# Performance work log

Hardware: AMD Instinct MI355X
Metric: run time of the kernel (lower is better)

## Reference

```python
import jax, jax.numpy as jnp
import numpy as np

NUM_HEAD = 16
NUM_SEQ = 2048
NUM_FEAT = 1024
HEAD_DIM = NUM_FEAT // NUM_HEAD
LN_EPS = 1e-5


def _constants():
    # decay per head: log(1 - 2^{-5-h})
    decay = jnp.log(1.0 - 2.0 ** (-5.0 - jnp.arange(NUM_HEAD, dtype=jnp.float32)))
    idx = jnp.arange(NUM_SEQ, dtype=jnp.float32)
    diff = idx[:, None] - idx[None, :]                      # [s, s]
    # exp(diff * decay) on lower triangle (incl. diagonal), 0 above
    mask = jnp.where(diff[None] >= 0, jnp.exp(diff[None] * decay[:, None, None]), 0.0)  # [h, s, s]
    # rotary angles: each frequency repeated twice
    angle = 1.0 / 10000.0 ** jnp.linspace(0.0, 1.0, HEAD_DIM // 2)
    angle = jnp.repeat(angle, 2)                            # [hd]
    sin = jnp.sin(idx[:, None] * angle[None, :])            # [s, hd]
    cos = jnp.cos(idx[:, None] * angle[None, :])
    return mask, sin, cos


def _rotate_every_two(x):
    x1 = x[..., ::2]
    x2 = x[..., 1::2]
    return jnp.stack((-x2, x1), axis=-1).reshape(x.shape)


def setup_inputs() -> dict:
    key = jax.random.key(0)
    ks = jax.random.split(key, 5)
    b, s, d = 4, NUM_SEQ, NUM_FEAT
    x = jax.random.normal(ks[0], (b, s, d), dtype=jnp.float32)
    Wq = jax.random.normal(ks[1], (d, d), dtype=jnp.float32) * 0.02
    Wk = jax.random.normal(ks[2], (d, d), dtype=jnp.float32) * 0.02
    Wv = jax.random.normal(ks[3], (d, d), dtype=jnp.float32) * 0.02
    Wo = jax.random.normal(ks[4], (d, d), dtype=jnp.float32) * 0.02
    ln_w = jnp.ones((HEAD_DIM,), dtype=jnp.float32)
    ln_b = jnp.zeros((HEAD_DIM,), dtype=jnp.float32)
    return {"x": x, "Wq": Wq, "Wk": Wk, "Wv": Wv, "Wo": Wo, "ln_w": ln_w, "ln_b": ln_b}


def reference(x, Wq, Wk, Wv, Wo, ln_w, ln_b):
    b, s, d = x.shape
    h, hd = NUM_HEAD, HEAD_DIM
    mask, sin, cos = _constants()

    def proj(W):
        # torch Linear (no bias): x @ W.T -> [b, h, s, hd]
        return (x @ W.T).reshape(b, s, h, hd).transpose(0, 2, 1, 3)

    q, k, v = proj(Wq), proj(Wk), proj(Wv)
    # rotary theta shift (sin/cos broadcast over batch & head)
    q = q * cos + _rotate_every_two(q) * sin
    k = k * cos + _rotate_every_two(k) * sin

    r = jnp.einsum('bhsd,bhtd->bhst', q, k) * mask[None]    # decay-masked scores
    o = jnp.einsum('bhst,bhtd->bhsd', r, v)                 # [b, h, s, hd]

    # LayerNorm over head_dim
    mu = jnp.mean(o, axis=-1, keepdims=True)
    var = jnp.var(o, axis=-1, keepdims=True)
    y = (o - mu) * jax.lax.rsqrt(var + LN_EPS) * ln_w + ln_b

    y = y.transpose(0, 2, 1, 3).reshape(b, s, d)
    return jax.nn.silu(y) @ Wo.T
```

## Files before the change

### kernel.cpp

```cpp
#include <hip/hip_runtime.h>
#include <math.h>

typedef unsigned short u16;
typedef __attribute__((ext_vector_type(8))) short short8;
typedef __attribute__((ext_vector_type(4))) float floatx4;

#define LDS_AS(p) ((__attribute__((address_space(3))) void*)(p))
#define GLB_AS(p) ((const __attribute__((address_space(1))) void*)(p))

__device__ __forceinline__ u16 f2bf(float f) {
  unsigned int u = __float_as_uint(f);
  u += 0x7fffu + ((u >> 16) & 1u);
  return (u16)(u >> 16);
}

__device__ __forceinline__ void gld16(const void* g, void* l) {
  __builtin_amdgcn_global_load_lds(GLB_AS(g), LDS_AS(l), 16, 0, 0);
}

__device__ __forceinline__ floatx4 mfma16(short8 a, short8 b, floatx4 c) {
  return __builtin_amdgcn_mfma_f32_16x16x32_bf16(a, b, c, 0, 0, 0);
}


__global__ void prep_kernel(const float* __restrict__ x, const float* __restrict__ Wq,
                            const float* __restrict__ Wk, const float* __restrict__ Wv,
                            const float* __restrict__ Wo, u16* __restrict__ xp,
                            u16* __restrict__ wqkvp, u16* __restrict__ wop,
                            float2* __restrict__ rtab) {
  int i = blockIdx.x * blockDim.x + threadIdx.x;
  const int str = gridDim.x * blockDim.x;
  for (; i < 3211264; i += str) {
    if (i < 3145728) {
      int U; u16* d;
      const float* s;
      if (i < 2097152)      { U = i;           d = xp;    s = x;  }
      else if (i < 2883584) { U = i - 2097152; d = wqkvp; s = nullptr; }
      else                  { U = i - 2883584; d = wop;   s = Wo; }
      const int tile = U >> 12;
      const int kc   = (U >> 7) & 31;
      const int lane = (U >> 1) & 63;
      const int jh   = U & 1;
      const int scol = kc * 32 + (lane >> 4) * 8 + jh * 4;
      int srow = tile * 16 + (lane & 15);
      if (s == nullptr) {
        const int sel = srow >> 10;
        srow &= 1023;
        s = (sel == 0) ? Wq : (sel == 1) ? Wk : Wv;
      }
      float4 v = ((const float4*)s)[srow * 256 + (scol >> 2)];
      ushort4 o;
      o.x = f2bf(v.x); o.y = f2bf(v.y); o.z = f2bf(v.z); o.w = f2bf(v.w);
      ((ushort4*)d)[U] = o;
    } else {
      const int t = i - 3145728;
      const int seq = t >> 5, dh = t & 31;
      const float freq = exp2f(-(float)dh * 0.42863594770f);
      float sn, cs;
      __sincosf((float)seq * freq, &sn, &cs);
      rtab[t] = make_float2(sn, cs);
    }
  }
}

template <int EPI>
__global__ __launch_bounds__(256, 2)
void gemm_bt(const u16* __restrict__ A, const u16* __restrict__ Bw, int K,
             u16* __restrict__ qb, u16* __restrict__ kb, u16* __restrict__ vtb,
             u16* __restrict__ kwt, const float2* __restrict__ rtab,
             float* __restrict__ outp) {
  constexpr int AP   = (EPI == 0) ? 8 : 4;
  constexpr int BUFU = (AP + 16) * 512;
  constexpr int AOFF = AP * 512;
  constexpr int AI   = (EPI == 0) ? 8 : 4;
  constexpr int IH   = (EPI == 0) ? 2 : 1;
  __shared__ __align__(16) u16 smem[3 * 12288];
  const int tid = threadIdx.x;
  const int w = tid >> 6, lane = tid & 63;
  const int quad = lane >> 4, l15 = lane & 15;
  const int m0 = blockIdx.y * (EPI == 0 ? 128 : 64), n0 = blockIdx.x * 256;

  const size_t tsz = (size_t)(K >> 5) * 512;
  const u16* A0 = A + ((size_t)(m0 >> 4) + (EPI == 0 ? 2 * w : w)) * tsz + lane * 8;
  const u16* A1 = A0 + tsz;
  const u16* Bb = Bw + ((size_t)(n0 >> 4) + 4 * w) * tsz + lane * 8;

  auto stage = [&](int buf, int kc) {
    const int nb = buf * BUFU;
    gld16(A0 + (size_t)kc * 512, &smem[nb + (EPI == 0 ? 2 * w : w) * 512]);
    if constexpr (EPI == 0)
      gld16(A1 + (size_t)kc * 512, &smem[nb + (2 * w + 1) * 512]);
#pragma unroll
    for (int e = 0; e < 4; ++e)
      gld16(Bb + (size_t)e * tsz + (size_t)kc * 512,
            &smem[nb + AOFF + (4 * w + e) * 512]);
  };

  floatx4 acc[AI][4] = {};
  const int NT = K >> 5;

  stage(0, 0);
  stage(1, 1);
  if constexpr (EPI == 0)
    asm volatile("s_waitcnt vmcnt(6)" ::: "memory");
  else
    asm volatile("s_waitcnt vmcnt(5)" ::: "memory");
  __builtin_amdgcn_s_barrier();

  int cur = 0, stg = 2;
  for (int t = 0; t < NT; ++t) {
    const u16* Ap = &smem[cur * BUFU];
    const u16* Bp = Ap + AOFF;
    short8 a[AI], b[4];
#pragma unroll
    for (int i = 0; i < AI; ++i)
      a[i] = *(const short8*)&Ap[i * 512 + lane * 8];
#pragma unroll
    for (int j = 0; j < 4; ++j)
      b[j] = *(const short8*)&Bp[(w * 4 + j) * 512 + lane * 8];
    if (t + 2 < NT) {
      stage(stg, t + 2);
      if constexpr (EPI == 0)
        asm volatile("s_waitcnt vmcnt(6)" ::: "memory");
      else
        asm volatile("s_waitcnt vmcnt(5)" ::: "memory");
    } else {
      asm volatile("s_waitcnt vmcnt(0)" ::: "memory");
    }
    __builtin_amdgcn_s_barrier();
    asm volatile("s_waitcnt lgkmcnt(0)" ::: "memory");
    __builtin_amdgcn_sched_barrier(0);
    __builtin_amdgcn_s_setprio(1);
#pragma unroll
    for (int i = 0; i < AI; ++i)
#pragma unroll
      for (int j = 0; j < 4; ++j)
        acc[i][j] = mfma16(a[i], b[j], acc[i][j]);
    __builtin_amdgcn_s_setprio(0);
    asm volatile("" ::: "memory");
    __builtin_amdgcn_s_barrier();
    asm volatile("" ::: "memory");
    cur = (cur == 2) ? 0 : cur + 1;
    stg = (stg == 2) ? 0 : stg + 1;
  }

  u16* scr = &smem[w * 4096];

  const int ncb = n0 + w * 64;

#pragma unroll
  for (int ih = 0; ih < IH; ++ih) {
    const int mrb = m0 + ih * 64;

    if (EPI == 0) {
      const int which = n0 >> 10;
      const int c1024 = ncb & 1023;
      const int bidx = mrb >> 11;
      const int hh = c1024 >> 6;
      const int seq0 = mrb & 2047;
      const int chk = seq0 >> 7;

      if (which < 2) {
#pragma unroll
        for (int j = 0; j < 4; ++j) {
          const int d = j * 16 + l15;
          const int dc = d >> 3, dl = d & 7;
#pragma unroll
          for (int i = 0; i < 4; ++i)
#pragma unroll
            for (int r = 0; r < 4; ++r) {
              const int sl = i * 16 + quad * 4 + r;
              const int seq = seq0 + sl;
              const float v = acc[ih * 4 + i][j][r];
              const float p = __shfl_xor(v, 1, 64);
              const float2 sc = rtab[(d >> 1) + seq * 32];
              const float res = (d & 1) ? (v * sc.y + p * sc.x) : (v * sc.y - p * sc.x);
              scr[sl * 64 + (((dc + (sl >> 2)) & 7) << 3) + dl] = f2bf(res);
            }
        }
        u16* dst = ((which == 0) ? qb : kb) +
                   (((size_t)(bidx * 16 + hh) * 16 + chk) << 13);
#pragma unroll
        for (int nl = 0; nl < 4; ++nl)
#pragma unroll
          for (int kk2 = 0; kk2 < 2; ++kk2) {
            const int slr = nl * 16 + l15;
            const int slot = ((kk2 * 4 + quad) + (slr >> 2)) & 7;
            short8 vv = *(const short8*)&scr[slr * 64 + slot * 8];
            *(short8*)(dst + (((ih * 4 + nl) * 2 + kk2) * 512) + lane * 8) = vv;
          }
        if (which == 1) {
          const float l2h = __log2f(1.0f - exp2f(-(float)(5 + hh)));
#pragma unroll
          for (int j = 0; j < 4; ++j) {
            const int d = j * 16 + l15;
#pragma unroll
            for (int i = 0; i < 4; ++i) {
              ushort4 pk;
#pragma unroll
              for (int r = 0; r < 4; ++r) {
                const int sl = i * 16 + quad * 4 + r;
                const int seq = seq0 + sl;
                const float v = acc[ih * 4 + i][j][r];
                const float p = __shfl_xor(v, 1, 64);
                const float2 sc = rtab[(d >> 1) + seq * 32];
                const float res = (d & 1) ? (v * sc.y + p * sc.x) : (v * sc.y - p * sc.x);
                const float wgt = exp2f((float)(127 - (seq & 127)) * l2h);
                ((u16*)&pk)[r] = f2bf(res * wgt);
              }
              *(ushort4*)&scr[d * 64 + ((i * 16 + quad * 4 + 8 * (d & 7)) & 63)] = pk;
            }
          }
          u16* dw = kwt + (((size_t)(bidx * 16 + hh) * 16 + chk) << 13);
#pragma unroll
          for (int m = 0; m < 4; ++m)
#pragma unroll
            for (int ks2 = 0; ks2 < 2; ++ks2) {
              const int dr = m * 16 + l15;
              const int col = ((ks2 * 32 + quad * 8) + 8 * (dr & 7)) & 63;
              short8 vv = *(const short8*)&scr[dr * 64 + col];
              *(short8*)(dw + ((m * 4 + ih * 2 + ks2) * 512) + lane * 8) = vv;
            }
        }
      } else {
#pragma unroll
        for (int j = 0; j < 4; ++j) {
          const int d = j * 16 + l15;
#pragma unroll
          for (int i = 0; i < 4; ++i) {
            ushort4 pk;
            pk.x = f2bf(acc[ih * 4 + i][j][0]);
            pk.y = f2bf(acc[ih * 4 + i][j][1]);
            pk.z = f2bf(acc[ih * 4 + i][j][2]);
            pk.w = f2bf(acc[ih * 4 + i][j][3]);
            *(ushort4*)&scr[d * 64 + ((i * 16 + quad * 4 + 8 * (d & 7)) & 63)] = pk;
          }
        }
        u16* dh = vtb + (((size_t)(bidx * 16 + hh) * 16 + chk) << 13);
#pragma unroll
        for (int m = 0; m < 4; ++m)
#pragma unroll
          for (int ks2 = 0; ks2 < 2; ++ks2) {
            const int dr = m * 16 + l15;
            const int col = ((ks2 * 32 + quad * 8) + 8 * (dr & 7)) & 63;
            short8 vv = *(const short8*)&scr[dr * 64 + col];
            *(short8*)(dh + ((m * 4 + ih * 2 + ks2) * 512) + lane * 8) = vv;
          }
      }
    } else {
      float* scrf = (float*)scr;
      const int lr4 = lane >> 4, lc16 = lane & 15;
#pragma unroll
      for (int p = 0; p < 4; ++p) {
#pragma unroll
        for (int j = 0; j < 4; ++j)
#pragma unroll
          for (int r = 0; r < 4; ++r)
            scrf[(quad * 4 + r) * 65 + j * 16 + l15] = acc[p][j][r];
#pragma unroll
        for (int cch = 0; cch < 4; ++cch) {
          const int rr = cch * 4 + lr4;
          float4 vv = *(const float4*)&scrf[rr * 65 + lc16 * 4];
          *(float4*)&outp[(size_t)(mrb + p * 16 + rr) * 1024 + ncb + lc16 * 4] = vv;
        }
      }
    }
  }
}

__global__ __launch_bounds__(256, 2)
void kvscan_kernel(const u16* __restrict__ kwt, const u16* __restrict__ vtb,
                   u16* __restrict__ Sb) {
  __shared__ __align__(16) u16 kls[2][16 * 512];
  __shared__ __align__(16) u16 vls[2][16 * 512];
  const int bh = blockIdx.x;
  const int tid = threadIdx.x, w = tid >> 6, lane = tid & 63;
  const int quad = lane >> 4, l15 = lane & 15;
  const int h = bh & 15;
  const float l2 = __log2f(1.0f - exp2f(-(float)(5 + h)));
  const float lamL = exp2f(128.0f * l2);

  const u16* kg = kwt + ((size_t)bh << 17);
  const u16* vg = vtb + ((size_t)bh << 17);
  u16* sbase = Sb + ((size_t)bh << 16);

  auto stage = [&](int buf, int c) {
    const u16* kc = kg + ((size_t)c << 13);
    const u16* vc = vg + ((size_t)c << 13);
#pragma unroll
    for (int rg = 0; rg < 4; ++rg) {
      const int rid = w * 4 + rg;
      gld16(kc + rid * 512 + lane * 8, &kls[buf][rid * 512]);
      gld16(vc + rid * 512 + lane * 8, &vls[buf][rid * 512]);
    }
  };

  float S[4][4] = {};

  stage(0, 0);
  int buf = 0;
  for (int c = 0; c < 16; ++c) {
    if (c + 1 < 16) {
      stage(buf ^ 1, c + 1);
      asm volatile("s_waitcnt vmcnt(8)" ::: "memory");
    } else {
      asm volatile("s_waitcnt vmcnt(0)" ::: "memory");
    }
    __builtin_amdgcn_s_barrier();
    asm volatile("" ::: "memory");

    u16* sp = sbase + ((size_t)c << 12);
#pragma unroll
    for (int m = 0; m < 4; ++m) {
      ushort4 pk;
#pragma unroll
      for (int r = 0; r < 4; ++r) ((u16*)&pk)[r] = f2bf(S[m][r]);
      const int lanep = ((m & 1) * 2 + (quad >> 1)) * 16 + l15;
      *(ushort4*)(sp + (w * 2 + (m >> 1)) * 512 + lanep * 8 + (quad & 1) * 4) = pk;
    }

    floatx4 acc[4] = {};
#pragma unroll
    for (int kst = 0; kst < 4; ++kst) {
      short8 bf = *(const short8*)&vls[buf][(w * 4 + kst) * 512 + lane * 8];
#pragma unroll
      for (int m = 0; m < 4; ++m) {
        short8 af = *(const short8*)&kls[buf][(m * 4 + kst) * 512 + lane * 8];
        acc[m] = mfma16(af, bf, acc[m]);
      }
    }
#pragma unroll
    for (int m = 0; m < 4; ++m)
#pragma unroll
      for (int r = 0; r < 4; ++r)
        S[m][r] = lamL * S[m][r] + acc[m][r];

    asm volatile("" ::: "memory");
    __builtin_amdgcn_s_barrier();
    buf ^= 1;
  }
}

__global__ __launch_bounds__(256, 2)
void attn_chunk_kernel(const u16* __restrict__ qb, const u16* __restrict__ kb,
                       const u16* __restrict__ vtb, const u16* __restrict__ Sb,
                       const float* __restrict__ lnw, const float* __restrict__ lnb,
                       u16* __restrict__ yb) {
  __shared__ __align__(16) u16 kls[16 * 512];
  __shared__ __align__(16) u16 vls[16 * 512];
  __shared__ __align__(16) u16 Sls[8 * 512];
  __shared__ __align__(16) u16 pls[4 * 32 * 40];

  const int c = blockIdx.x, bh = blockIdx.y, h = bh & 15;
  const int tid = threadIdx.x;
  const int w = tid >> 6, lane = tid & 63, quad = lane >> 4, l15 = lane & 15;
  const float l2 = __log2f(1.0f - exp2f(-(float)(5 + h)));

  const u16* kg = kb + (((size_t)bh * 16 + c) << 13);
  const u16* vg = vtb + (((size_t)bh * 16 + c) << 13);
  const u16* Sg = Sb + (((size_t)bh * 16 + c) << 12);
#pragma unroll
  for (int rg = 0; rg < 4; ++rg) {
    const int kid = w * 4 + rg;
    gld16(kg + kid * 512 + lane * 8, &kls[kid * 512]);
    gld16(vg + kid * 512 + lane * 8, &vls[kid * 512]);
  }
#pragma unroll
  for (int e = 0; e < 2; ++e) {
    const int rid = w * 2 + e;
    gld16(Sg + rid * 512 + lane * 8, &Sls[rid * 512]);
  }

  short8 qf[2][2];
  {
    const u16* qp = qb + (((size_t)bh * 16 + c) << 13);
#pragma unroll
    for (int i = 0; i < 2; ++i)
#pragma unroll
      for (int kk = 0; kk < 2; ++kk)
        qf[i][kk] = *(const short8*)(qp + (((w * 2 + i) * 2 + kk) * 512) + lane * 8);
  }
  float lnwv[4], lnbv[4];
#pragma unroll
  for (int jd = 0; jd < 4; ++jd) {
    lnwv[jd] = lnw[jd * 16 + l15];
    lnbv[jd] = lnb[jd * 16 + l15];
  }
  __syncthreads();

  floatx4 sacc[2][8] = {};
#pragma unroll
  for (int kk = 0; kk < 2; ++kk) {
    short8 bf[8];
#pragma unroll
    for (int j = 0; j < 8; ++j)
      bf[j] = *(const short8*)&kls[(j * 2 + kk) * 512 + lane * 8];
#pragma unroll
    for (int i = 0; i < 2; ++i)
#pragma unroll
      for (int j = 0; j < 8; ++j)
        sacc[i][j] = mfma16(qf[i][kk], bf[j], sacc[i][j]);
  }

  floatx4 oacc[2][4] = {};
#pragma unroll
  for (int kk = 0; kk < 2; ++kk)
#pragma unroll
    for (int nd = 0; nd < 4; ++nd) {
      short8 sf = *(const short8*)&Sls[(nd * 2 + kk) * 512 + lane * 8];
#pragma unroll
      for (int i = 0; i < 2; ++i)
        oacc[i][nd] = mfma16(qf[i][kk], sf, oacc[i][nd]);
    }
  float rowf[8];
#pragma unroll
  for (int i = 0; i < 2; ++i)
#pragma unroll
    for (int r = 0; r < 4; ++r)
      rowf[i * 4 + r] = exp2f((float)(w * 32 + i * 16 + quad * 4 + r) * l2);
  const float lam1 = exp2f(l2);
#pragma unroll
  for (int i = 0; i < 2; ++i)
#pragma unroll
    for (int nd = 0; nd < 4; ++nd)
#pragma unroll
      for (int r = 0; r < 4; ++r)
        oacc[i][nd][r] *= rowf[i * 4 + r] * lam1;

  float colf[8];
#pragma unroll
  for (int j = 0; j < 8; ++j) colf[j] = exp2f(-(float)(j * 16 + l15) * l2);
  u16* pw = &pls[w * 1280];
#pragma unroll
  for (int kst = 0; kst < 4; ++kst) {
#pragma unroll
    for (int jl = 0; jl < 2; ++jl) {
      const int j = kst * 2 + jl;
#pragma unroll
      for (int i = 0; i < 2; ++i)
#pragma unroll
        for (int r = 0; r < 4; ++r) {
          const int srow = i * 16 + quad * 4 + r;
          const int dlt = (w * 32 + srow) - (j * 16 + l15);
          const float v =
              (dlt >= 0) ? sacc[i][j][r] * rowf[i * 4 + r] * colf[j] : 0.0f;
          pw[srow * 40 + jl * 16 + l15] = f2bf(v);
        }
    }
    short8 pf[2], vf[4];
#pragma unroll
    for (int i = 0; i < 2; ++i)
      pf[i] = *(const short8*)&pw[(i * 16 + l15) * 40 + quad * 8];
#pragma unroll
    for (int jd = 0; jd < 4; ++jd)
      vf[jd] = *(const short8*)&vls[(jd * 4 + kst) * 512 + lane * 8];
#pragma unroll
    for (int i = 0; i < 2; ++i)
#pragma unroll
      for (int jd = 0; jd < 4; ++jd)
        oacc[i][jd] = mfma16(pf[i], vf[jd], oacc[i][jd]);
  }

  __syncthreads();
  u16* scrw = &kls[w * 2048];
  const int b = bh >> 4;
#pragma unroll
  for (int i = 0; i < 2; ++i)
#pragma unroll
    for (int r = 0; r < 4; ++r) {
      float sum = 0.f, ssq = 0.f;
#pragma unroll
      for (int jd = 0; jd < 4; ++jd) {
        const float v = oacc[i][jd][r];
        sum += v;
        ssq += v * v;
      }
#pragma unroll
      for (int off = 1; off < 16; off <<= 1) {
        sum += __shfl_xor(sum, off, 64);
        ssq += __shfl_xor(ssq, off, 64);
      }
      const float mu = sum * (1.0f / 64.0f);
      const float var = ssq * (1.0f / 64.0f) - mu * mu;
      const float rst = rsqrtf(var + 1e-5f);
      const int sl = i * 16 + quad * 4 + r;
#pragma unroll
      for (int jd = 0; jd < 4; ++jd) {
        const float z = (oacc[i][jd][r] - mu) * rst * lnwv[jd] + lnbv[jd];
        const float y = z / (1.0f + expf(-z));
        const int f = jd * 16 + l15;
        scrw[sl * 64 + ((((f >> 3) + (sl >> 2)) & 7) << 3) + (f & 7)] = f2bf(y);
      }
    }
  const int tile0 = b * 128 + c * 8 + w * 2;
#pragma unroll
  for (int tt = 0; tt < 2; ++tt)
#pragma unroll
    for (int kcl = 0; kcl < 2; ++kcl) {
      const int row = tt * 16 + l15;
      const int slot = ((kcl * 4 + quad) + (row >> 2)) & 7;
      short8 vv = *(const short8*)&scrw[row * 64 + slot * 8];
      *(short8*)(yb + ((size_t)(tile0 + tt) * 32 + h * 2 + kcl) * 512 + lane * 8) = vv;
    }
}

extern "C" void kernel_launch(void* const* d_in, const int* in_sizes, int n_in,
                              void* d_out, int out_size, void* d_ws, size_t ws_size,
                              hipStream_t stream) {
  const float* x   = (const float*)d_in[0];
  const float* Wq  = (const float*)d_in[1];
  const float* Wk  = (const float*)d_in[2];
  const float* Wv  = (const float*)d_in[3];
  const float* Wo  = (const float*)d_in[4];
  const float* lnw = (const float*)d_in[5];
  const float* lnb = (const float*)d_in[6];
  float* out = (float*)d_out;

  char* ws = (char*)d_ws;
  u16* xbf  = (u16*)(ws + 0);
  u16* wqkv = (u16*)(ws + 16777216);
  u16* Sb   = (u16*)(ws + 16777216);
  u16* qbuf = (u16*)(ws + 25165824);
  u16* kbuf = (u16*)(ws + 41943040);
  u16* vtb  = (u16*)(ws + 58720256);
  u16* wo   = (u16*)(ws + 75497472);
  float2* rtab = (float2*)(ws + 77594624);
  u16* yb   = xbf;
  u16* kwt  = (u16*)d_out;

  prep_kernel<<<dim3(1024), dim3(256), 0, stream>>>(x, Wq, Wk, Wv, Wo, xbf, wqkv, wo,
                                                    rtab);
  gemm_bt<0><<<dim3(12, 64), dim3(256), 0, stream>>>(xbf, wqkv, 1024, qbuf, kbuf, vtb,
                                                     kwt, rtab, nullptr);
  kvscan_kernel<<<dim3(64), dim3(256), 0, stream>>>(kwt, vtb, Sb);
  attn_chunk_kernel<<<dim3(16, 64), dim3(256), 0, stream>>>(qbuf, kbuf, vtb, Sb, lnw,
                                                            lnb, yb);
  gemm_bt<1><<<dim3(4, 128), dim3(256), 0, stream>>>(yb, wo, 1024, nullptr, nullptr,
                                                     nullptr, nullptr, nullptr, out);
}
```

Measured before the change: 236.3 us.

## Add dedicated 256x256-tile QKV GEMM with 8 waves and interleaved staging

Replaces the templated QKV projection GEMM (128x256 tiles, 4 waves, 3-stage buffer) with a dedicated kernel using 256x256 tiles, 512 threads, K-steps of 64 with double buffering, and global-to-LDS loads spread across four sub-steps of the MFMA loop. The larger tile raises arithmetic intensity and halves the grid, and the interleaved staging is meant to hide load latency behind compute. The 128KB of LDS per block and the larger register footprint limit occupancy, and fewer blocks (384) may leave CUs underfilled. The output-projection GEMM is simplified to its single epilogue path.

```diff
diff --git a/kernel.cpp b/kernel.cpp
--- a/kernel.cpp
+++ b/kernel.cpp
@@ -63,33 +63,214 @@
   }
 }
 
+__global__ __launch_bounds__(512, 2)
+void gemm_qkv(const u16* __restrict__ A, const u16* __restrict__ Bw,
+              u16* __restrict__ qb, u16* __restrict__ kb, u16* __restrict__ vtb,
+              u16* __restrict__ kwt, const float2* __restrict__ rtab) {
+  __shared__ __align__(16) u16 smem[65536];
+  const int tid = threadIdx.x;
+  const int w = tid >> 6, lane = tid & 63;
+  const int quad = lane >> 4, l15 = lane & 15;
+  const int wr = w >> 2, wc = w & 3;
+  const int m0 = blockIdx.y * 256, n0 = blockIdx.x * 256;
+  constexpr int NT = 16;
+  const size_t tsz = (size_t)32 * 512;
+
+  auto stageA = [&](int buf, int t, int half) {
+    const int rt = (w & 3) + (w >> 2) * 8 + half * 4;
+    const u16* src = A + ((size_t)(m0 >> 4) + rt) * tsz + (size_t)(2 * t) * 512 + lane * 8;
+    u16* dst = &smem[buf * 32768 + rt * 1024];
+    gld16(src, dst);
+    gld16(src + 512, dst + 512);
+  };
+  auto stageB = [&](int buf, int t, int half) {
+    const int ct = half * 8 + w;
+    const u16* src = Bw + ((size_t)(n0 >> 4) + ct) * tsz + (size_t)(2 * t) * 512 + lane * 8;
+    u16* dst = &smem[buf * 32768 + 16384 + ct * 1024];
+    gld16(src, dst);
+    gld16(src + 512, dst + 512);
+  };
+
+  floatx4 acc[8][4] = {};
+
+  stageB(0, 0, 0); stageB(0, 0, 1); stageA(0, 0, 0); stageA(0, 0, 1);
+  stageB(1, 1, 0); stageB(1, 1, 1); stageA(1, 1, 0);
+  asm volatile("s_waitcnt vmcnt(6)" ::: "memory");
+  __builtin_amdgcn_s_barrier();
+
+  for (int t = 0; t < NT; ++t) {
+    const int bb = (t & 1) * 32768;
+    const u16* Ap = &smem[bb];
+    const u16* Bp = &smem[bb + 16384];
+    short8 b[4][2];
+#pragma unroll
+    for (int j = 0; j < 4; ++j)
+#pragma unroll
+      for (int kk = 0; kk < 2; ++kk)
+        b[j][kk] = *(const short8*)&Bp[((wc * 4 + j) * 2 + kk) * 512 + lane * 8];
+#pragma unroll
+    for (int q = 0; q < 4; ++q) {
+      short8 a[2][2];
+#pragma unroll
+      for (int i = 0; i < 2; ++i)
+#pragma unroll
+        for (int kk = 0; kk < 2; ++kk)
+          a[i][kk] =
+              *(const short8*)&Ap[((wr * 8 + q * 2 + i) * 2 + kk) * 512 + lane * 8];
+      if (q == 0) {
+        if (t + 1 < NT) stageA((t + 1) & 1, t + 1, 1);
+      } else if (q == 1) {
+        if (t + 2 < NT) stageB(t & 1, t + 2, 0);
+      } else if (q == 2) {
+        if (t + 2 < NT) stageB(t & 1, t + 2, 1);
+      } else {
+        if (t + 2 < NT) stageA(t & 1, t + 2, 0);
+        if (t <= NT - 3)
+          asm volatile("s_waitcnt vmcnt(6)" ::: "memory");
+        else
+          asm volatile("s_waitcnt vmcnt(0)" ::: "memory");
+      }
+      __builtin_amdgcn_s_barrier();
+      asm volatile("s_waitcnt lgkmcnt(0)" ::: "memory");
+      __builtin_amdgcn_sched_barrier(0);
+      __builtin_amdgcn_s_setprio(1);
+#pragma unroll
+      for (int i = 0; i < 2; ++i)
+#pragma unroll
+        for (int j = 0; j < 4; ++j)
+#pragma unroll
+          for (int kk = 0; kk < 2; ++kk)
+            acc[q * 2 + i][j] = mfma16(a[i][kk], b[j][kk], acc[q * 2 + i][j]);
+      __builtin_amdgcn_s_setprio(0);
+      asm volatile("" ::: "memory");
+      __builtin_amdgcn_s_barrier();
+      asm volatile("" ::: "memory");
+    }
+  }
+
+  u16* scr = &smem[w * 4096];
+  const int ncb = n0 + wc * 64;
+  const int which = n0 >> 10;
+  const int hh = (ncb & 1023) >> 6;
+
+#pragma unroll
+  for (int ih = 0; ih < 2; ++ih) {
+    const int mrb = m0 + wr * 128 + ih * 64;
+    const int bidx = mrb >> 11;
+    const int seq0 = mrb & 2047;
+    const int chk = seq0 >> 7;
+
+    if (which < 2) {
+#pragma unroll
+      for (int j = 0; j < 4; ++j) {
+        const int d = j * 16 + l15;
+        const int dc = d >> 3, dl = d & 7;
+#pragma unroll
+        for (int i = 0; i < 4; ++i)
+#pragma unroll
+          for (int r = 0; r < 4; ++r) {
+            const int sl = i * 16 + quad * 4 + r;
+            const int seq = seq0 + sl;
+            const float v = acc[ih * 4 + i][j][r];
+            const float p = __shfl_xor(v, 1, 64);
+            const float2 sc = rtab[(d >> 1) + seq * 32];
+            const float res = (d & 1) ? (v * sc.y + p * sc.x) : (v * sc.y - p * sc.x);
+            scr[sl * 64 + (((dc + (sl >> 2)) & 7) << 3) + dl] = f2bf(res);
+          }
+      }
+      u16* dst = ((which == 0) ? qb : kb) +
+                 (((size_t)(bidx * 16 + hh) * 16 + chk) << 13);
+#pragma unroll
+      for (int nl = 0; nl < 4; ++nl)
+#pragma unroll
+        for (int kk2 = 0; kk2 < 2; ++kk2) {
+          const int slr = nl * 16 + l15;
+          const int slot = ((kk2 * 4 + quad) + (slr >> 2)) & 7;
+          short8 vv = *(const short8*)&scr[slr * 64 + slot * 8];
+          *(short8*)(dst + (((ih * 4 + nl) * 2 + kk2) * 512) + lane * 8) = vv;
+        }
+      if (which == 1) {
+        const float l2h = __log2f(1.0f - exp2f(-(float)(5 + hh)));
+#pragma unroll
+        for (int j = 0; j < 4; ++j) {
+          const int d = j * 16 + l15;
+#pragma unroll
+          for (int i = 0; i < 4; ++i) {
+            ushort4 pk;
+#pragma unroll
+            for (int r = 0; r < 4; ++r) {
+              const int sl = i * 16 + quad * 4 + r;
+              const int seq = seq0 + sl;
+              const float v = acc[ih * 4 + i][j][r];
+              const float p = __shfl_xor(v, 1, 64);
+              const float2 sc = rtab[(d >> 1) + seq * 32];
+              const float res = (d & 1) ? (v * sc.y + p * sc.x) : (v * sc.y - p * sc.x);
+              const float wgt = exp2f((float)(127 - (seq & 127)) * l2h);
+              ((u16*)&pk)[r] = f2bf(res * wgt);
+            }
+            *(ushort4*)&scr[d * 64 + ((i * 16 + quad * 4 + 8 * (d & 7)) & 63)] = pk;
+          }
+        }
+        u16* dw = kwt + (((size_t)(bidx * 16 + hh) * 16 + chk) << 13);
+#pragma unroll
+        for (int m = 0; m < 4; ++m)
+#pragma unroll
+          for (int ks2 = 0; ks2 < 2; ++ks2) {
+            const int dr = m * 16 + l15;
+            const int col = ((ks2 * 32 + quad * 8) + 8 * (dr & 7)) & 63;
+            short8 vv = *(const short8*)&scr[dr * 64 + col];
+            *(short8*)(dw + ((m * 4 + ih * 2 + ks2) * 512) + lane * 8) = vv;
+          }
+      }
+    } else {
+#pragma unroll
+      for (int j = 0; j < 4; ++j) {
+        const int d = j * 16 + l15;
+#pragma unroll
+        for (int i = 0; i < 4; ++i) {
+          ushort4 pk;
+          pk.x = f2bf(acc[ih * 4 + i][j][0]);
+          pk.y = f2bf(acc[ih * 4 + i][j][1]);
+          pk.z = f2bf(acc[ih * 4 + i][j][2]);
+          pk.w = f2bf(acc[ih * 4 + i][j][3]);
+          *(ushort4*)&scr[d * 64 + ((i * 16 + quad * 4 + 8 * (d & 7)) & 63)] = pk;
+        }
+      }
+      u16* dh = vtb + (((size_t)(bidx * 16 + hh) * 16 + chk) << 13);
+#pragma unroll
+      for (int m = 0; m < 4; ++m)
+#pragma unroll
+        for (int ks2 = 0; ks2 < 2; ++ks2) {
+          const int dr = m * 16 + l15;
+          const int col = ((ks2 * 32 + quad * 8) + 8 * (dr & 7)) & 63;
+          short8 vv = *(const short8*)&scr[dr * 64 + col];
+          *(short8*)(dh + ((m * 4 + ih * 2 + ks2) * 512) + lane * 8) = vv;
+        }
+    }
+  }
+}
+
 template <int EPI>
 __global__ __launch_bounds__(256, 2)
 void gemm_bt(const u16* __restrict__ A, const u16* __restrict__ Bw, int K,
-             u16* __restrict__ qb, u16* __restrict__ kb, u16* __restrict__ vtb,
-             u16* __restrict__ kwt, const float2* __restrict__ rtab,
-             float* __restrict__ outp) {
-  constexpr int AP   = (EPI == 0) ? 8 : 4;
+             const float2* __restrict__ rtab, float* __restrict__ outp) {
+  constexpr int AP   = 4;
   constexpr int BUFU = (AP + 16) * 512;
   constexpr int AOFF = AP * 512;
-  constexpr int AI   = (EPI == 0) ? 8 : 4;
-  constexpr int IH   = (EPI == 0) ? 2 : 1;
+  constexpr int AI   = 4;
   __shared__ __align__(16) u16 smem[3 * 12288];
   const int tid = threadIdx.x;
   const int w = tid >> 6, lane = tid & 63;
   const int quad = lane >> 4, l15 = lane & 15;
-  const int m0 = blockIdx.y * (EPI == 0 ? 128 : 64), n0 = blockIdx.x * 256;
+  const int m0 = blockIdx.y * 64, n0 = blockIdx.x * 256;
 
   const size_t tsz = (size_t)(K >> 5) * 512;
-  const u16* A0 = A + ((size_t)(m0 >> 4) + (EPI == 0 ? 2 * w : w)) * tsz + lane * 8;
-  const u16* A1 = A0 + tsz;
+  const u16* A0 = A + ((size_t)(m0 >> 4) + w) * tsz + lane * 8;
   const u16* Bb = Bw + ((size_t)(n0 >> 4) + 4 * w) * tsz + lane * 8;
 
   auto stage = [&](int buf, int kc) {
     const int nb = buf * BUFU;
-    gld16(A0 + (size_t)kc * 512, &smem[nb + (EPI == 0 ? 2 * w : w) * 512]);
-    if constexpr (EPI == 0)
-      gld16(A1 + (size_t)kc * 512, &smem[nb + (2 * w + 1) * 512]);
+    gld16(A0 + (size_t)kc * 512, &smem[nb + w * 512]);
 #pragma unroll
     for (int e = 0; e < 4; ++e)
       gld16(Bb + (size_t)e * tsz + (size_t)kc * 512,
@@ -101,10 +282,7 @@
 
   stage(0, 0);
   stage(1, 1);
-  if constexpr (EPI == 0)
-    asm volatile("s_waitcnt vmcnt(6)" ::: "memory");
-  else
-    asm volatile("s_waitcnt vmcnt(5)" ::: "memory");
+  asm volatile("s_waitcnt vmcnt(5)" ::: "memory");
   __builtin_amdgcn_s_barrier();
 
   int cur = 0, stg = 2;
@@ -120,10 +298,7 @@
       b[j] = *(const short8*)&Bp[(w * 4 + j) * 512 + lane * 8];
     if (t + 2 < NT) {
       stage(stg, t + 2);
-      if constexpr (EPI == 0)
-        asm volatile("s_waitcnt vmcnt(6)" ::: "memory");
-      else
-        asm volatile("s_waitcnt vmcnt(5)" ::: "memory");
+      asm volatile("s_waitcnt vmcnt(5)" ::: "memory");
     } else {
       asm volatile("s_waitcnt vmcnt(0)" ::: "memory");
     }
@@ -145,125 +320,22 @@
   }
 
   u16* scr = &smem[w * 4096];
-
   const int ncb = n0 + w * 64;
-
-#pragma unroll
-  for (int ih = 0; ih < IH; ++ih) {
-    const int mrb = m0 + ih * 64;
-
-    if (EPI == 0) {
-      const int which = n0 >> 10;
-      const int c1024 = ncb & 1023;
-      const int bidx = mrb >> 11;
-      const int hh = c1024 >> 6;
-      const int seq0 = mrb & 2047;
-      const int chk = seq0 >> 7;
-
-      if (which < 2) {
-#pragma unroll
-        for (int j = 0; j < 4; ++j) {
-          const int d = j * 16 + l15;
-          const int dc = d >> 3, dl = d & 7;
-#pragma unroll
-          for (int i = 0; i < 4; ++i)
-#pragma unroll
-            for (int r = 0; r < 4; ++r) {
-              const int sl = i * 16 + quad * 4 + r;
-              const int seq = seq0 + sl;
-              const float v = acc[ih * 4 + i][j][r];
-              const float p = __shfl_xor(v, 1, 64);
-              const float2 sc = rtab[(d >> 1) + seq * 32];
-              const float res = (d & 1) ? (v * sc.y + p * sc.x) : (v * sc.y - p * sc.x);
-              scr[sl * 64 + (((dc + (sl >> 2)) & 7) << 3) + dl] = f2bf(res);
-            }
-        }
-        u16* dst = ((which == 0) ? qb : kb) +
-                   (((size_t)(bidx * 16 + hh) * 16 + chk) << 13);
-#pragma unroll
-        for (int nl = 0; nl < 4; ++nl)
-#pragma unroll
-          for (int kk2 = 0; kk2 < 2; ++kk2) {
-            const int slr = nl * 16 + l15;
-            const int slot = ((kk2 * 4 + quad) + (slr >> 2)) & 7;
-            short8 vv = *(const short8*)&scr[slr * 64 + slot * 8];
-            *(short8*)(dst + (((ih * 4 + nl) * 2 + kk2) * 512) + lane * 8) = vv;
-          }
-        if (which == 1) {
-          const float l2h = __log2f(1.0f - exp2f(-(float)(5 + hh)));
-#pragma unroll
-          for (int j = 0; j < 4; ++j) {
-            const int d = j * 16 + l15;
-#pragma unroll
-            for (int i = 0; i < 4; ++i) {
-              ushort4 pk;
-#pragma unroll
-              for (int r = 0; r < 4; ++r) {
-                const int sl = i * 16 + quad * 4 + r;
-                const int seq = seq0 + sl;
-                const float v = acc[ih * 4 + i][j][r];
-                const float p = __shfl_xor(v, 1, 64);
-                const float2 sc = rtab[(d >> 1) + seq * 32];
-                const float res = (d & 1) ? (v * sc.y + p * sc.x) : (v * sc.y - p * sc.x);
-                const float wgt = exp2f((float)(127 - (seq & 127)) * l2h);
-                ((u16*)&pk)[r] = f2bf(res * wgt);
-              }
-              *(ushort4*)&scr[d * 64 + ((i * 16 + quad * 4 + 8 * (d & 7)) & 63)] = pk;
-            }
-          }
-          u16* dw = kwt + (((size_t)(bidx * 16 + hh) * 16 + chk) << 13);
-#pragma unroll
-          for (int m = 0; m < 4; ++m)
-#pragma unroll
-            for (int ks2 = 0; ks2 < 2; ++ks2) {
-              const int dr = m * 16 + l15;
-              const int col = ((ks2 * 32 + quad * 8) + 8 * (dr & 7)) & 63;
-              short8 vv = *(const short8*)&scr[dr * 64 + col];
-              *(short8*)(dw + ((m * 4 + ih * 2 + ks2) * 512) + lane * 8) = vv;
-            }
-        }
-      } else {
-#pragma unroll
-        for (int j = 0; j < 4; ++j) {
-          const int d = j * 16 + l15;
-#pragma unroll
-          for (int i = 0; i < 4; ++i) {
-            ushort4 pk;
-            pk.x = f2bf(acc[ih * 4 + i][j][0]);
-            pk.y = f2bf(acc[ih * 4 + i][j][1]);
-            pk.z = f2bf(acc[ih * 4 + i][j][2]);
-            pk.w = f2bf(acc[ih * 4 + i][j][3]);
-            *(ushort4*)&scr[d * 64 + ((i * 16 + quad * 4 + 8 * (d & 7)) & 63)] = pk;
-          }
-        }
-        u16* dh = vtb + (((size_t)(bidx * 16 + hh) * 16 + chk) << 13);
-#pragma unroll
-        for (int m = 0; m < 4; ++m)
-#pragma unroll
-          for (int ks2 = 0; ks2 < 2; ++ks2) {
-            const int dr = m * 16 + l15;
-            const int col = ((ks2 * 32 + quad * 8) + 8 * (dr & 7)) & 63;
-            short8 vv = *(const short8*)&scr[dr * 64 + col];
-            *(short8*)(dh + ((m * 4 + ih * 2 + ks2) * 512) + lane * 8) = vv;
-          }
-      }
-    } else {
-      float* scrf = (float*)scr;
-      const int lr4 = lane >> 4, lc16 = lane & 15;
-#pragma unroll
-      for (int p = 0; p < 4; ++p) {
-#pragma unroll
-        for (int j = 0; j < 4; ++j)
-#pragma unroll
-          for (int r = 0; r < 4; ++r)
-            scrf[(quad * 4 + r) * 65 + j * 16 + l15] = acc[p][j][r];
-#pragma unroll
-        for (int cch = 0; cch < 4; ++cch) {
-          const int rr = cch * 4 + lr4;
-          float4 vv = *(const float4*)&scrf[rr * 65 + lc16 * 4];
-          *(float4*)&outp[(size_t)(mrb + p * 16 + rr) * 1024 + ncb + lc16 * 4] = vv;
-        }
-      }
+  const int mrb = m0;
+  float* scrf = (float*)scr;
+  const int lr4 = lane >> 4, lc16 = lane & 15;
+#pragma unroll
+  for (int p = 0; p < 4; ++p) {
+#pragma unroll
+    for (int j = 0; j < 4; ++j)
+#pragma unroll
+      for (int r = 0; r < 4; ++r)
+        scrf[(quad * 4 + r) * 65 + j * 16 + l15] = acc[p][j][r];
+#pragma unroll
+    for (int cch = 0; cch < 4; ++cch) {
+      const int rr = cch * 4 + lr4;
+      float4 vv = *(const float4*)&scrf[rr * 65 + lc16 * 4];
+      *(float4*)&outp[(size_t)(mrb + p * 16 + rr) * 1024 + ncb + lc16 * 4] = vv;
     }
   }
 }
@@ -530,11 +602,10 @@
 
   prep_kernel<<<dim3(1024), dim3(256), 0, stream>>>(x, Wq, Wk, Wv, Wo, xbf, wqkv, wo,
                                                     rtab);
-  gemm_bt<0><<<dim3(12, 64), dim3(256), 0, stream>>>(xbf, wqkv, 1024, qbuf, kbuf, vtb,
-                                                     kwt, rtab, nullptr);
+  gemm_qkv<<<dim3(12, 32), dim3(512), 0, stream>>>(xbf, wqkv, qbuf, kbuf, vtb, kwt,
+                                                   rtab);
   kvscan_kernel<<<dim3(64), dim3(256), 0, stream>>>(kwt, vtb, Sb);
   attn_chunk_kernel<<<dim3(16, 64), dim3(256), 0, stream>>>(qbuf, kbuf, vtb, Sb, lnw,
                                                             lnb, yb);
-  gemm_bt<1><<<dim3(4, 128), dim3(256), 0, stream>>>(yb, wo, 1024, nullptr, nullptr,
-                                                     nullptr, nullptr, nullptr, out);
-}
+  gemm_bt<1><<<dim3(4, 128), dim3(256), 0, stream>>>(yb, wo, 1024, rtab, out);
+}
```

New measurement: 256.5 us. 1.09x slower.
